# Optimization experiments

Measured on AMD Instinct MI355X. Metric: run time of the kernel, lower is better.

Reference implementation:

```python
import jax, jax.numpy as jnp
import numpy as np

EPS = 1e-5
INV_SQRT2 = 0.7071067811865476

def _rmsnorm(x, w):
    rms = jnp.sqrt(jnp.sum(x * x, axis=-1) / x.shape[-1] + EPS)
    return x / rms[..., None] * w

def _gelu(x):
    # exact erf-based GELU as in the torch module
    return x * (1.0 + jax.scipy.special.erf(x * INV_SQRT2)) * 0.5

def setup_inputs() -> dict:
    key = jax.random.key(0)
    ks = jax.random.split(key, 8)
    B, S, D, DFF = 4, 2048, 1024, 4096
    s = 0.02  # realistic init scale keeps softmax non-degenerate
    return {
        "x": jax.random.normal(ks[0], (B, S, D), jnp.float32),
        "ln1": jax.random.uniform(ks[1], (D,), jnp.float32),
        "ln2": jax.random.uniform(ks[2], (D,), jnp.float32),
        "ffn1": jax.random.normal(ks[3], (DFF, D), jnp.float32) * s,
        "ffn2": jax.random.normal(ks[4], (D, DFF), jnp.float32) * s,
        "k_proj": jax.random.normal(ks[5], (D, D), jnp.float32) * s,
        "q_proj": jax.random.normal(ks[6], (D, D), jnp.float32) * s,
        "v_proj": jax.random.normal(ks[7], (D, D), jnp.float32) * s,
        "out_proj": jax.random.normal(jax.random.fold_in(key, 99), (D, D), jnp.float32) * s,
    }

def reference(x, ln1, ln2, ffn1, ffn2, k_proj, q_proj, v_proj, out_proj):
    S = x.shape[1]
    d_k = x.shape[-1]
    # --- attention branch (single-head, as in source) ---
    h = _rmsnorm(x, ln1)
    Q = h @ q_proj.T  # [B,S,D]
    K = h @ k_proj.T
    V = h @ v_proj.T
    scores = jnp.einsum('bqd,bkd->bqk', Q, K) / jnp.sqrt(jnp.float32(d_k))
    attn = jax.nn.softmax(scores, axis=-1)
    # source: softmax first, then zero out strict-upper (future) entries, renormalize
    causal = jnp.tril(jnp.ones((S, S), jnp.float32))
    attn = attn * causal
    attn = attn / jnp.sum(attn, axis=-1, keepdims=True)
    mh = jnp.einsum('bqk,bkd->bqd', attn, V) @ out_proj
    y = x + mh
    # --- FFN branch: NOTE source feeds RMSNorm2(x), not y ---
    h2 = _rmsnorm(x, ln2)
    ff = _gelu(h2 @ ffn1.T) @ ffn2.T
    return y + ff
```

## Files before the change

kernel.cpp:

```cpp
#include <hip/hip_runtime.h>
#include <math.h>

typedef __bf16 bf16_t;
typedef __bf16 bf16x8 __attribute__((ext_vector_type(8)));
typedef float f32x4 __attribute__((ext_vector_type(4)));

#define LDS16(g, l) __builtin_amdgcn_global_load_lds( \
    (__attribute__((address_space(1))) void*)(g),     \
    (__attribute__((address_space(3))) void*)(l), 16, 0, 0)

__global__ __launch_bounds__(256) void prep_kernel(
    const float* __restrict__ qp, const float* __restrict__ kp,
    const float* __restrict__ vp, const float* __restrict__ f1,
    const float* __restrict__ f2, const float* __restrict__ op,
    const float* __restrict__ x, const float* __restrict__ ln1,
    bf16_t* __restrict__ qkvb, bf16_t* __restrict__ f1b,
    bf16_t* __restrict__ f2b, bf16_t* __restrict__ opT,
    bf16_t* __restrict__ h1)
{
    __shared__ float tile[32][33];
    __shared__ float red[4];
    int bid = blockIdx.x;
    int t = threadIdx.x;
    if (bid < 11264) {
        size_t i = ((size_t)bid * 256 + t) * 4;
        const float* src;
        bf16_t* dst;
        if (i < 3145728) {
            if (i < 1048576)      { src = qp + i;             dst = qkvb + i; }
            else if (i < 2097152) { src = kp + (i - 1048576); dst = qkvb + i; }
            else                  { src = vp + (i - 2097152); dst = qkvb + i; }
        } else if (i < 7340032) { src = f1 + (i - 3145728); dst = f1b + (i - 3145728); }
        else                    { src = f2 + (i - 7340032); dst = f2b + (i - 7340032); }
        float4 v = *(const float4*)src;
        dst[0] = (bf16_t)v.x; dst[1] = (bf16_t)v.y;
        dst[2] = (bf16_t)v.z; dst[3] = (bf16_t)v.w;
    } else if (bid < 12288) {
        int b2 = bid - 11264;
        int c0 = (b2 & 31) * 32, r0 = (b2 >> 5) * 32;
        int tx = t & 31, ty = t >> 5;
#pragma unroll
        for (int i = 0; i < 32; i += 8)
            tile[ty + i][tx] = op[(size_t)(r0 + ty + i) * 1024 + c0 + tx];
        __syncthreads();
#pragma unroll
        for (int i = 0; i < 32; i += 8)
            opT[(size_t)(c0 + ty + i) * 1024 + r0 + tx] = (bf16_t)tile[tx][ty + i];
    } else {
        int row = bid - 12288;
        float4 xv = ((const float4*)(x + (size_t)row * 1024))[t];
        float ss = xv.x * xv.x + xv.y * xv.y + xv.z * xv.z + xv.w * xv.w;
#pragma unroll
        for (int o = 32; o > 0; o >>= 1) ss += __shfl_xor(ss, o, 64);
        if ((t & 63) == 0) red[t >> 6] = ss;
        __syncthreads();
        ss = red[0] + red[1] + red[2] + red[3];
        float rinv = rsqrtf(ss * (1.0f / 1024.0f) + 1e-5f);
        float4 wv = ((const float4*)ln1)[t];
        bf16_t* hp = h1 + (size_t)row * 1024 + t * 4;
        hp[0] = (bf16_t)(xv.x * rinv * wv.x);
        hp[1] = (bf16_t)(xv.y * rinv * wv.y);
        hp[2] = (bf16_t)(xv.z * rinv * wv.z);
        hp[3] = (bf16_t)(xv.w * rinv * wv.w);
    }
}

__global__ __launch_bounds__(256) void rmsnorm_kernel(
    const float* __restrict__ x, const float* __restrict__ w,
    bf16_t* __restrict__ h)
{
    int row = blockIdx.x;
    int t = threadIdx.x;
    float4 xv = ((const float4*)(x + (size_t)row * 1024))[t];
    float ss = xv.x * xv.x + xv.y * xv.y + xv.z * xv.z + xv.w * xv.w;
#pragma unroll
    for (int o = 32; o > 0; o >>= 1) ss += __shfl_xor(ss, o, 64);
    __shared__ float red[4];
    if ((t & 63) == 0) red[t >> 6] = ss;
    __syncthreads();
    ss = red[0] + red[1] + red[2] + red[3];
    float rinv = rsqrtf(ss * (1.0f / 1024.0f) + 1e-5f);
    float4 wv = ((const float4*)w)[t];
    bf16_t* hp = h + (size_t)row * 1024 + t * 4;
    hp[0] = (bf16_t)(xv.x * rinv * wv.x);
    hp[1] = (bf16_t)(xv.y * rinv * wv.y);
    hp[2] = (bf16_t)(xv.z * rinv * wv.z);
    hp[3] = (bf16_t)(xv.w * rinv * wv.w);
}

__global__ __launch_bounds__(256) void transpose_bf16(
    const bf16_t* __restrict__ in, bf16_t* __restrict__ out,
    int rows, int ldin, long long sIn, long long sOut)
{
    __shared__ bf16_t tile[32][33];
    int b = blockIdx.z;
    const bf16_t* ip = in + (long long)b * sIn;
    bf16_t* op = out + (long long)b * sOut;
    int c0 = blockIdx.x * 32, r0 = blockIdx.y * 32;
    int tx = threadIdx.x & 31, ty = threadIdx.x >> 5;
#pragma unroll
    for (int i = 0; i < 32; i += 8)
        tile[ty + i][tx] = ip[(size_t)(r0 + ty + i) * ldin + c0 + tx];
    __syncthreads();
#pragma unroll
    for (int i = 0; i < 32; i += 8)
        op[(size_t)(c0 + ty + i) * rows + r0 + tx] = tile[tx][ty + i];
}

__global__ __launch_bounds__(256) void causal_softmax_kernel(bf16_t* __restrict__ SP)
{
    const int S = 2048;
    int q = blockIdx.x, b = blockIdx.y;
    bf16_t* row = SP + ((size_t)b * S + q) * S;
    int t = threadIdx.x;
    int j0 = t * 8;
    int Jstore = ((q >> 7) + 1) << 7;

    float v[8];
    if (j0 + 7 <= q) {
        bf16x8 xv = *(const bf16x8*)(row + j0);
#pragma unroll
        for (int i = 0; i < 8; i++) v[i] = (float)xv[i];
    } else if (j0 <= q) {
#pragma unroll
        for (int i = 0; i < 8; i++)
            v[i] = (j0 + i <= q) ? (float)row[j0 + i] : -1e30f;
    } else {
#pragma unroll
        for (int i = 0; i < 8; i++) v[i] = -1e30f;
    }

    float mx = v[0];
#pragma unroll
    for (int i = 1; i < 8; i++) mx = fmaxf(mx, v[i]);
#pragma unroll
    for (int o = 32; o > 0; o >>= 1) mx = fmaxf(mx, __shfl_xor(mx, o, 64));
    __shared__ float sm[4], ssum[4];
    if ((t & 63) == 0) sm[t >> 6] = mx;
    __syncthreads();
    mx = fmaxf(fmaxf(sm[0], sm[1]), fmaxf(sm[2], sm[3]));

    float e[8];
    float sum = 0.f;
#pragma unroll
    for (int i = 0; i < 8; i++) {
        e[i] = (v[i] > -1e29f) ? expf(v[i] - mx) : 0.f;
        sum += e[i];
    }
#pragma unroll
    for (int o = 32; o > 0; o >>= 1) sum += __shfl_xor(sum, o, 64);
    if ((t & 63) == 0) ssum[t >> 6] = sum;
    __syncthreads();
    sum = ssum[0] + ssum[1] + ssum[2] + ssum[3];
    float r = 1.0f / sum;

    if (j0 < Jstore) {
        bf16x8 ov;
#pragma unroll
        for (int i = 0; i < 8; i++) ov[i] = (bf16_t)(e[i] * r);
        *(bf16x8*)(row + j0) = ov;
    }
}

template <int EPI, bool CSKIP, bool CKLOOP, bool ASPLIT>
__global__ __launch_bounds__(256) void gemm_bt(
    const bf16_t* __restrict__ A, const bf16_t* __restrict__ A2, int lda,
    const bf16_t* __restrict__ B, int ldb,
    void* Cv, int ldc, const float* R,
    int K, int Ksp, int Mt, long long sA, long long sB, long long sC,
    float scale)
{
    int id = blockIdx.x, bz = blockIdx.z;
    int xcd = id & 7, p = id >> 3;
    int chunk = Mt >> 3;
    int bm = xcd * chunk + (p % chunk);
    int bn = p / chunk;
    if (CSKIP && bn > bm) return;

    __shared__ __align__(16) bf16_t At[128 * 64];
    __shared__ __align__(16) bf16_t Bt[128 * 64];
    int t = threadIdx.x;
    int w = t >> 6, l = t & 63;
    int wm = w >> 1, wn = w & 1;
    int lane_m = l & 15, quad = l >> 4;

    const bf16_t* Ag = A + (long long)bz * sA + (size_t)(bm * 128) * lda;
    const bf16_t* Bg = B + (long long)bz * sB + (size_t)(bn * 128) * ldb;

    int Keff = K;
    if (CKLOOP) {
        int kk = (bm + 1) * 128;
        if (kk < K) Keff = kk;
    }

    f32x4 acc[4][4] = {};

    int rb = w * 8 + (l >> 3);
    int g0 = ((l & 7) ^ ((l >> 3) & 7)) * 8;
    const bf16_t* a0[4];
    const bf16_t* a1[4];
    const bf16_t* b0[4];
#pragma unroll
    for (int j = 0; j < 4; j++) {
        size_t ro = (size_t)(rb + 32 * j);
        a0[j] = Ag + ro * lda + g0;
        if (ASPLIT) a1[j] = A2 + (long long)bz * sA + (size_t)(bm * 128) * lda
                           + ro * lda + g0;
        b0[j] = Bg + ro * ldb + g0;
    }

    int s0 = (quad ^ (lane_m & 7)) * 8;
    int s1 = ((4 + quad) ^ (lane_m & 7)) * 8;

    for (int kt = 0; kt < Keff; kt += 64) {
        __syncthreads();
#pragma unroll
        for (int j = 0; j < 4; j++) {
            const bf16_t* pa = a0[j] + kt;
            if (ASPLIT && kt >= Ksp) pa = a1[j] + (kt - Ksp);
            LDS16(pa, At + (size_t)w * 512 + j * 2048);
            LDS16(b0[j] + kt, Bt + (size_t)w * 512 + j * 2048);
        }
        __syncthreads();

#pragma unroll
        for (int h = 0; h < 2; h++) {
            int sh = h ? s1 : s0;
            bf16x8 af[4], bfr[4];
#pragma unroll
            for (int mi = 0; mi < 4; mi++)
                af[mi] = *(const bf16x8*)(At + (wm * 64 + mi * 16 + lane_m) * 64 + sh);
#pragma unroll
            for (int ni = 0; ni < 4; ni++)
                bfr[ni] = *(const bf16x8*)(Bt + (wn * 64 + ni * 16 + lane_m) * 64 + sh);
#pragma unroll
            for (int mi = 0; mi < 4; mi++)
#pragma unroll
                for (int ni = 0; ni < 4; ni++)
                    acc[mi][ni] = __builtin_amdgcn_mfma_f32_16x16x32_bf16(
                        af[mi], bfr[ni], acc[mi][ni], 0, 0, 0);
        }
    }

    long long cbase = (long long)bz * sC;
#pragma unroll
    for (int mi = 0; mi < 4; mi++) {
#pragma unroll
        for (int r = 0; r < 4; r++) {
            int row = bm * 128 + wm * 64 + mi * 16 + quad * 4 + r;
#pragma unroll
            for (int ni = 0; ni < 4; ni++) {
                int col = bn * 128 + wn * 64 + ni * 16 + lane_m;
                float v = acc[mi][ni][r];
                size_t idx = (size_t)(cbase + (long long)row * ldc + col);
                if (EPI == 0) {
                    ((bf16_t*)Cv)[idx] = (bf16_t)(v * scale);
                } else if (EPI == 1) {
                    float g = 0.5f * v * (1.0f + erff(v * 0.70710678118654752f));
                    ((bf16_t*)Cv)[idx] = (bf16_t)g;
                } else {
                    float rv = R[(size_t)row * ldc + col];
                    ((float*)Cv)[idx] = v + rv;
                }
            }
        }
    }
}

#define VM8 asm volatile("s_waitcnt vmcnt(8)" ::: "memory")
#define VM4 asm volatile("s_waitcnt vmcnt(4)" ::: "memory")
#define VM0 asm volatile("s_waitcnt vmcnt(0)" ::: "memory")
#define NOP ((void)0)

#define STAGE_A(BUF, KH, KOFF) do { \
    LDS16(rA0 + (KOFF), &As[BUF][KH][w * 512]);        \
    LDS16(rA1 + (KOFF), &As[BUF][KH][4096 + w * 512]); } while (0)
#define STAGE_B(BUF, KH, KOFF) do { \
    LDS16(rB0 + (KOFF), &Bs[BUF][KH][w * 512]);        \
    LDS16(rB1 + (KOFF), &Bs[BUF][KH][4096 + w * 512]); } while (0)

#define PHASE(BUF, KH, MQ, STAGE_STMT, WAIT_STMT)                             \
  {                                                                           \
    _Pragma("unroll") for (int mi = 0; mi < 4; mi++)                          \
        af[mi] = *(const bf16x8*)&As[BUF][KH][arow + (MQ)*2048 + mi*512];     \
    if ((MQ) == 0) {                                                          \
      _Pragma("unroll") for (int ni = 0; ni < 4; ni++)                        \
          bfr[ni] = *(const bf16x8*)&Bs[BUF][KH][brow + ni*512];              \
    }                                                                         \
    STAGE_STMT;                                                               \
    __builtin_amdgcn_s_barrier();                                             \
    asm volatile("s_waitcnt lgkmcnt(0)" ::: "memory");                        \
    __builtin_amdgcn_sched_barrier(0);                                        \
    __builtin_amdgcn_s_setprio(1);                                            \
    _Pragma("unroll") for (int mi = 0; mi < 4; mi++)                          \
      _Pragma("unroll") for (int ni = 0; ni < 4; ni++)                        \
        acc[(MQ)*4 + mi][ni] = __builtin_amdgcn_mfma_f32_16x16x32_bf16(       \
            af[mi], bfr[ni], acc[(MQ)*4 + mi][ni], 0, 0, 0);                  \
    __builtin_amdgcn_s_setprio(0);                                            \
    WAIT_STMT;                                                                \
    __builtin_amdgcn_s_barrier();                                             \
  }

template <int EPI>
__global__ __launch_bounds__(512, 2) void gemm256(
    const bf16_t* __restrict__ A, int lda,
    const bf16_t* __restrict__ B, int ldb,
    void* Cv, int ldc, const float* R, int K, int Nt, float scale)
{
    int id = blockIdx.x;
    int xcd = id & 7, p = id >> 3;
    int chunk = gridDim.x >> 3;
    int g = xcd * chunk + p;
    int bm = g / Nt, bn = g % Nt;

    __shared__ __align__(16) bf16_t As[2][2][256 * 32];
    __shared__ __align__(16) bf16_t Bs[2][2][256 * 32];

    int t = threadIdx.x;
    int w = t >> 6, l = t & 63;
    int wm = w >> 2, wn = w & 3;
    int lm = l & 15, quad = l >> 4;

    const bf16_t* Ag = A + (size_t)(bm * 256) * lda;
    const bf16_t* Bg = B + (size_t)(bn * 256) * ldb;

    int g4 = ((l & 3) ^ ((l >> 2) & 3)) * 8;
    const bf16_t* rA0 = Ag + (size_t)(w * 16 + (l >> 2)) * lda + g4;
    const bf16_t* rA1 = rA0 + (size_t)128 * lda;
    const bf16_t* rB0 = Bg + (size_t)(w * 16 + (l >> 2)) * ldb + g4;
    const bf16_t* rB1 = rB0 + (size_t)128 * ldb;

    int slot8 = (quad ^ (lm & 3)) * 8;
    int arow = (wm * 128 + lm) * 32 + slot8;
    int brow = (wn * 64 + lm) * 32 + slot8;

    f32x4 acc[8][4] = {};
    bf16x8 af[4], bfr[4];

    STAGE_A(0, 0, 0);  STAGE_B(0, 0, 0);
    STAGE_A(0, 1, 32); STAGE_B(0, 1, 32);
    STAGE_A(1, 0, 64); STAGE_B(1, 0, 64);
    VM8;
    __builtin_amdgcn_s_barrier();

    int T = K >> 7;
    for (int it = 0; it < T - 1; ++it) {
        int kb = it << 7;
        PHASE(0, 0, 0, STAGE_A(1, 1, kb + 96),  NOP);
        PHASE(0, 0, 1, STAGE_B(1, 1, kb + 96),  VM8);
        PHASE(0, 1, 0, STAGE_A(0, 0, kb + 128), NOP);
        PHASE(0, 1, 1, STAGE_B(0, 0, kb + 128), VM8);
        PHASE(1, 0, 0, STAGE_A(0, 1, kb + 160), NOP);
        PHASE(1, 0, 1, STAGE_B(0, 1, kb + 160), VM8);
        PHASE(1, 1, 0, STAGE_A(1, 0, kb + 192), NOP);
        PHASE(1, 1, 1, STAGE_B(1, 0, kb + 192), VM8);
    }
    {
        int kb = (T - 1) << 7;
        PHASE(0, 0, 0, STAGE_A(1, 1, kb + 96), NOP);
        PHASE(0, 0, 1, STAGE_B(1, 1, kb + 96), VM8);
        PHASE(0, 1, 0, NOP, NOP);
        PHASE(0, 1, 1, NOP, VM4);
        PHASE(1, 0, 0, NOP, NOP);
        PHASE(1, 0, 1, NOP, VM0);
        PHASE(1, 1, 0, NOP, NOP);
        PHASE(1, 1, 1, NOP, NOP);
    }

#pragma unroll
    for (int mq = 0; mq < 2; mq++) {
#pragma unroll
        for (int mi = 0; mi < 4; mi++) {
#pragma unroll
            for (int r = 0; r < 4; r++) {
                int row = bm * 256 + wm * 128 + mq * 64 + mi * 16 + quad * 4 + r;
#pragma unroll
                for (int ni = 0; ni < 4; ni++) {
                    int col = bn * 256 + wn * 64 + ni * 16 + lm;
                    float v = acc[mq * 4 + mi][ni][r];
                    size_t idx = (size_t)row * ldc + col;
                    if (EPI == 0) {
                        ((bf16_t*)Cv)[idx] = (bf16_t)(v * scale);
                    } else if (EPI == 1) {
                        float ge = 0.5f * v * (1.0f + erff(v * 0.70710678118654752f));
                        ((bf16_t*)Cv)[idx] = (bf16_t)ge;
                    } else {
                        float rv = R[(size_t)row * ldc + col];
                        ((float*)Cv)[idx] = v + rv;
                    }
                }
            }
        }
    }
}

extern "C" void kernel_launch(void* const* d_in, const int* in_sizes, int n_in,
                              void* d_out, int out_size, void* d_ws, size_t ws_size,
                              hipStream_t stream)
{
    (void)in_sizes; (void)n_in; (void)out_size;
    const float* x    = (const float*)d_in[0];
    const float* ln1  = (const float*)d_in[1];
    const float* ln2  = (const float*)d_in[2];
    const float* ffn1 = (const float*)d_in[3];
    const float* ffn2 = (const float*)d_in[4];
    const float* kp   = (const float*)d_in[5];
    const float* qp   = (const float*)d_in[6];
    const float* vp   = (const float*)d_in[7];
    const float* op   = (const float*)d_in[8];
    float* out = (float*)d_out;

    const size_t MiB = 1048576;
    char* ws = (char*)d_ws;
    bf16_t* qkvb = (bf16_t*)(ws + 0 * MiB);
    bf16_t* opT  = (bf16_t*)(ws + 6 * MiB);
    bf16_t* f1b  = (bf16_t*)(ws + 8 * MiB);
    bf16_t* f2b  = (bf16_t*)(ws + 16 * MiB);
    bf16_t* h1   = (bf16_t*)(ws + 24 * MiB);
    bf16_t* VT   = (bf16_t*)(ws + 24 * MiB);
    bf16_t* h2   = (bf16_t*)(ws + 24 * MiB);
    bf16_t* QKVb = (bf16_t*)(ws + 40 * MiB);
    bf16_t* AV   = (bf16_t*)(ws + 40 * MiB);
    bf16_t* G0   = (bf16_t*)(ws + 40 * MiB);
    bf16_t* SP   = (bf16_t*)d_out;
    bool bigws = ws_size >= 104 * MiB;

    dim3 blk(256);
    dim3 blk5(512);
    const int HUGE_K = 1 << 30;

    prep_kernel<<<dim3(20480), blk, 0, stream>>>(
        qp, kp, vp, ffn1, ffn2, op, x, ln1, qkvb, f1b, f2b, opT, h1);

    gemm256<0><<<dim3(384), blk5, 0, stream>>>(
        h1, 1024, qkvb, 1024, QKVb, 3072, nullptr, 1024, 12, 1.0f);

    gemm_bt<0, true, false, false><<<dim3(256, 1, 4), blk, 0, stream>>>(
        QKVb, QKVb, 3072, QKVb + 1024, 3072, SP, 2048, nullptr,
        1024, HUGE_K, 16,
        (long long)2048 * 3072, (long long)2048 * 3072, (long long)2048 * 2048,
        1.0f / 32.0f);

    transpose_bf16<<<dim3(32, 64, 4), blk, 0, stream>>>(
        QKVb + 2048, VT, 2048, 3072,
        (long long)2048 * 3072, (long long)1024 * 2048);

    causal_softmax_kernel<<<dim3(2048, 4), blk, 0, stream>>>(SP);

    gemm_bt<0, false, true, false><<<dim3(128, 1, 4), blk, 0, stream>>>(
        SP, SP, 2048, VT, 2048, AV, 1024, nullptr,
        2048, HUGE_K, 16,
        (long long)2048 * 2048, (long long)1024 * 2048, (long long)2048 * 1024,
        1.0f);

    gemm256<2><<<dim3(128), blk5, 0, stream>>>(
        AV, 1024, opT, 1024, out, 1024, x, 1024, 4, 1.0f);

    rmsnorm_kernel<<<dim3(8192), blk, 0, stream>>>(x, ln2, h2);

    if (bigws) {
        gemm256<1><<<dim3(512), blk5, 0, stream>>>(
            h2, 1024, f1b, 1024, G0, 4096, nullptr, 1024, 16, 1.0f);
        gemm256<2><<<dim3(128), blk5, 0, stream>>>(
            G0, 4096, f2b, 4096, out, 1024, out, 4096, 4, 1.0f);
    } else {
        for (int half = 0; half < 2; half++) {
            gemm_bt<1, false, false, false><<<dim3(1024), blk, 0, stream>>>(
                h2, h2, 1024, f1b + (size_t)half * 2048 * 1024, 1024, G0, 2048,
                nullptr, 1024, HUGE_K, 64, 0, 0, 0, 1.0f);
            gemm_bt<2, false, false, false><<<dim3(512), blk, 0, stream>>>(
                G0, G0, 2048, f2b + half * 2048, 4096, out, 1024, out,
                2048, HUGE_K, 64, 0, 0, 0, 1.0f);
        }
    }
}
```

Baseline: 595.2 us.

## Fuse RMSNorm2 into prep, retune LDS swizzle, switch several GEMMs to gemm_bt

The second RMSNorm is computed inside the prep kernel from the same x row and sum of squares, which removes a separate rmsnorm launch when the workspace is large. The QKV, out-projection and FFN2 GEMMs move from the 256-tile 512-thread kernel to the smaller-tile gemm_bt kernel with more blocks, which may improve occupancy or wave balance for these shapes. The gemm256 LDS swizzle pattern is changed, presumably to cut bank conflicts, and softmax uses the fast __expf. Workspace offsets are reshuffled so h2 lives in a separate region, which requires the large workspace.

```diff
diff --git a/kernel.cpp b/kernel.cpp
--- a/kernel.cpp
+++ b/kernel.cpp
@@ -14,9 +14,10 @@
     const float* __restrict__ vp, const float* __restrict__ f1,
     const float* __restrict__ f2, const float* __restrict__ op,
     const float* __restrict__ x, const float* __restrict__ ln1,
+    const float* __restrict__ ln2,
     bf16_t* __restrict__ qkvb, bf16_t* __restrict__ f1b,
     bf16_t* __restrict__ f2b, bf16_t* __restrict__ opT,
-    bf16_t* __restrict__ h1)
+    bf16_t* __restrict__ h1, bf16_t* h2p)
 {
     __shared__ float tile[32][33];
     __shared__ float red[4];
@@ -56,12 +57,20 @@
         __syncthreads();
         ss = red[0] + red[1] + red[2] + red[3];
         float rinv = rsqrtf(ss * (1.0f / 1024.0f) + 1e-5f);
-        float4 wv = ((const float4*)ln1)[t];
+        float4 w1 = ((const float4*)ln1)[t];
         bf16_t* hp = h1 + (size_t)row * 1024 + t * 4;
-        hp[0] = (bf16_t)(xv.x * rinv * wv.x);
-        hp[1] = (bf16_t)(xv.y * rinv * wv.y);
-        hp[2] = (bf16_t)(xv.z * rinv * wv.z);
-        hp[3] = (bf16_t)(xv.w * rinv * wv.w);
+        hp[0] = (bf16_t)(xv.x * rinv * w1.x);
+        hp[1] = (bf16_t)(xv.y * rinv * w1.y);
+        hp[2] = (bf16_t)(xv.z * rinv * w1.z);
+        hp[3] = (bf16_t)(xv.w * rinv * w1.w);
+        if (h2p) {
+            float4 w2 = ((const float4*)ln2)[t];
+            bf16_t* hq = h2p + (size_t)row * 1024 + t * 4;
+            hq[0] = (bf16_t)(xv.x * rinv * w2.x);
+            hq[1] = (bf16_t)(xv.y * rinv * w2.y);
+            hq[2] = (bf16_t)(xv.z * rinv * w2.z);
+            hq[3] = (bf16_t)(xv.w * rinv * w2.w);
+        }
     }
 }
 
@@ -144,7 +153,7 @@
     float sum = 0.f;
 #pragma unroll
     for (int i = 0; i < 8; i++) {
-        e[i] = (v[i] > -1e29f) ? expf(v[i] - mx) : 0.f;
+        e[i] = (v[i] > -1e29f) ? __expf(v[i] - mx) : 0.f;
         sum += e[i];
     }
 #pragma unroll
@@ -324,13 +333,13 @@
     const bf16_t* Ag = A + (size_t)(bm * 256) * lda;
     const bf16_t* Bg = B + (size_t)(bn * 256) * ldb;
 
-    int g4 = ((l & 3) ^ ((l >> 2) & 3)) * 8;
+    int g4 = ((l & 3) ^ ((l >> 3) & 3)) * 8;
     const bf16_t* rA0 = Ag + (size_t)(w * 16 + (l >> 2)) * lda + g4;
     const bf16_t* rA1 = rA0 + (size_t)128 * lda;
     const bf16_t* rB0 = Bg + (size_t)(w * 16 + (l >> 2)) * ldb + g4;
     const bf16_t* rB1 = rB0 + (size_t)128 * ldb;
 
-    int slot8 = (quad ^ (lm & 3)) * 8;
+    int slot8 = (quad ^ ((lm >> 1) & 3)) * 8;
     int arow = (wm * 128 + lm) * 32 + slot8;
     int brow = (wn * 64 + lm) * 32 + slot8;
 
@@ -418,10 +427,10 @@
     bf16_t* f2b  = (bf16_t*)(ws + 16 * MiB);
     bf16_t* h1   = (bf16_t*)(ws + 24 * MiB);
     bf16_t* VT   = (bf16_t*)(ws + 24 * MiB);
-    bf16_t* h2   = (bf16_t*)(ws + 24 * MiB);
     bf16_t* QKVb = (bf16_t*)(ws + 40 * MiB);
     bf16_t* AV   = (bf16_t*)(ws + 40 * MiB);
-    bf16_t* G0   = (bf16_t*)(ws + 40 * MiB);
+    bf16_t* h2   = (bf16_t*)(ws + 88 * MiB);
+    bf16_t* G0   = (bf16_t*)(ws + 24 * MiB);
     bf16_t* SP   = (bf16_t*)d_out;
     bool bigws = ws_size >= 104 * MiB;
 
@@ -430,10 +439,12 @@
     const int HUGE_K = 1 << 30;
 
     prep_kernel<<<dim3(20480), blk, 0, stream>>>(
-        qp, kp, vp, ffn1, ffn2, op, x, ln1, qkvb, f1b, f2b, opT, h1);
-
-    gemm256<0><<<dim3(384), blk5, 0, stream>>>(
-        h1, 1024, qkvb, 1024, QKVb, 3072, nullptr, 1024, 12, 1.0f);
+        qp, kp, vp, ffn1, ffn2, op, x, ln1, ln2,
+        qkvb, f1b, f2b, opT, h1, bigws ? h2 : (bf16_t*)nullptr);
+
+    gemm_bt<0, false, false, false><<<dim3(1536), blk, 0, stream>>>(
+        h1, h1, 1024, qkvb, 1024, QKVb, 3072, nullptr,
+        1024, HUGE_K, 64, 0, 0, 0, 1.0f);
 
     gemm_bt<0, true, false, false><<<dim3(256, 1, 4), blk, 0, stream>>>(
         QKVb, QKVb, 3072, QKVb + 1024, 3072, SP, 2048, nullptr,
@@ -453,23 +464,26 @@
         (long long)2048 * 2048, (long long)1024 * 2048, (long long)2048 * 1024,
         1.0f);
 
-    gemm256<2><<<dim3(128), blk5, 0, stream>>>(
-        AV, 1024, opT, 1024, out, 1024, x, 1024, 4, 1.0f);
-
-    rmsnorm_kernel<<<dim3(8192), blk, 0, stream>>>(x, ln2, h2);
+    gemm_bt<2, false, false, false><<<dim3(512), blk, 0, stream>>>(
+        AV, AV, 1024, opT, 1024, out, 1024, x,
+        1024, HUGE_K, 64, 0, 0, 0, 1.0f);
 
     if (bigws) {
         gemm256<1><<<dim3(512), blk5, 0, stream>>>(
             h2, 1024, f1b, 1024, G0, 4096, nullptr, 1024, 16, 1.0f);
-        gemm256<2><<<dim3(128), blk5, 0, stream>>>(
-            G0, 4096, f2b, 4096, out, 1024, out, 4096, 4, 1.0f);
+        gemm_bt<2, false, false, false><<<dim3(512), blk, 0, stream>>>(
+            G0, G0, 4096, f2b, 4096, out, 1024, out,
+            4096, HUGE_K, 64, 0, 0, 0, 1.0f);
     } else {
+        bf16_t* h2s = (bf16_t*)(ws + 24 * MiB);
+        bf16_t* G0s = (bf16_t*)(ws + 40 * MiB);
+        rmsnorm_kernel<<<dim3(8192), blk, 0, stream>>>(x, ln2, h2s);
         for (int half = 0; half < 2; half++) {
             gemm_bt<1, false, false, false><<<dim3(1024), blk, 0, stream>>>(
-                h2, h2, 1024, f1b + (size_t)half * 2048 * 1024, 1024, G0, 2048,
+                h2s, h2s, 1024, f1b + (size_t)half * 2048 * 1024, 1024, G0s, 2048,
                 nullptr, 1024, HUGE_K, 64, 0, 0, 0, 1.0f);
             gemm_bt<2, false, false, false><<<dim3(512), blk, 0, stream>>>(
-                G0, G0, 2048, f2b + half * 2048, 4096, out, 1024, out,
+                G0s, G0s, 2048, f2b + half * 2048, 4096, out, 1024, out,
                 2048, HUGE_K, 64, 0, 0, 0, 1.0f);
         }
     }
```

New measurement: 520.9 us. -12.5%, faster.
